# Kernel optimization log

Hardware: AMD Instinct MI355X
Metric: run time of the kernel (lower is better)

The kernel has to match this reference:

```python
import jax, jax.numpy as jnp
import numpy as np

B, T, C = 16, 1024, 32
PATCH_SIZE = 4
NB_PATCHES = 400
STRETCH = 8
K = PATCH_SIZE * C          # patch_size * num_channels = 128
S_MAIN = T // STRETCH       # 128 strided steps for the main layer
P_TOP = max(int(0.15 * NB_PATCHES), PATCH_SIZE - 1)  # 60 ontop patches


def setup_inputs() -> dict:
    key = jax.random.key(0)
    k0, k1, k2, k3, k4 = jax.random.split(key, 5)
    x = jax.random.normal(k0, (B, T, C), dtype=jnp.float32)
    # flattened (time*C + channel) gather indices, stand-in for the
    # precomputed random (time, channel) pairs used by tf.gather_nd
    idx_main = jax.random.randint(k1, (S_MAIN, NB_PATCHES, K), 0, T * C, dtype=jnp.int32)
    idx_top = jax.random.randint(k2, (T, P_TOP, K), 0, T * C, dtype=jnp.int32)
    W_main = jax.random.normal(k3, (S_MAIN, NB_PATCHES, K), dtype=jnp.float32) * 0.05
    b_main = jnp.zeros((S_MAIN, NB_PATCHES), dtype=jnp.float32)
    W_top = jax.random.normal(k4, (T, P_TOP, K), dtype=jnp.float32) * 0.05
    b_top = jnp.zeros((T, P_TOP), dtype=jnp.float32)
    return {"x": x, "W_main": W_main, "b_main": b_main,
            "W_top": W_top, "b_top": b_top,
            "idx_main": idx_main, "idx_top": idx_top}


def reference(x, W_main, b_main, W_top, b_top, idx_main, idx_top):
    # x: [B, T, C] -> flatten time/channel plane for gather (== gather_nd on [T, C, B])
    Bsz, Tlen, Cch = x.shape
    flat = x.reshape(Bsz, Tlen * Cch)                      # [B, T*C]
    # main strided patches: [B, S_MAIN, NB_PATCHES, K]
    Mm = jnp.take(flat, idx_main.reshape(-1), axis=1).reshape(Bsz, *idx_main.shape)
    out_main = jax.nn.leaky_relu(
        jnp.einsum('bspk,spk->bsp', Mm, W_main) + b_main, 0.3)  # [B, S_MAIN, P]
    # upsample strided steps back to full sequence (tf_repeat along time)
    stretch = Tlen // idx_main.shape[0]
    out_main = jnp.repeat(out_main, stretch, axis=1)            # [B, T, P]
    # ontop patches at every step: [B, T, P_TOP, K]
    Mt = jnp.take(flat, idx_top.reshape(-1), axis=1).reshape(Bsz, *idx_top.shape)
    out_top = jax.nn.leaky_relu(
        jnp.einsum('btpk,tpk->btp', Mt, W_top) + b_top, 0.3)    # [B, T, P_TOP]
    return jnp.concatenate([out_main, out_top], axis=-1)       # [B, T, P + P_TOP]
```

## Files before the change

### kernel.cpp

```cpp
#include <hip/hip_runtime.h>

#define B_SZ    16
#define T_LEN   1024
#define C_CH    32
#define TC      (T_LEN * C_CH)
#define S_MAIN  128
#define NB_P    400
#define P_TOP   60
#define KDIM    128
#define STRETCH 8
#define OUT_CH  (NB_P + P_TOP)

__global__ __launch_bounds__(256) void transpose_x(const float* __restrict__ x,
                                                   float* __restrict__ xT) {
    __shared__ float tile[16][129];
    const int i0 = blockIdx.x * 128;
    const int t  = threadIdx.x;
    #pragma unroll
    for (int r = 0; r < 8; ++r) {
        int e  = r * 256 + t;
        int b  = e >> 7;
        int ii = e & 127;
        tile[b][ii] = x[b * TC + i0 + ii];
    }
    __syncthreads();
    #pragma unroll
    for (int r = 0; r < 8; ++r) {
        int e  = r * 256 + t;
        int ii = e >> 4;
        int b  = e & 15;
        xT[i0 * 16 + e] = tile[b][ii];
    }
}

__device__ __forceinline__ float4 fma4(float4 a, float s, float4 g) {
    a.x += g.x * s; a.y += g.y * s; a.z += g.z * s; a.w += g.w * s;
    return a;
}

template <int NPAIR_P, int NROWS, bool TO_WS>
__global__ __launch_bounds__(256) void patch_kernel(
    const float* __restrict__ xT,
    const int*   __restrict__ idx,
    const float* __restrict__ W,
    const float* __restrict__ bias,
    float*       __restrict__ dst)
{
    const int wave = threadIdx.x >> 6;
    const int lane = threadIdx.x & 63;
    const int pair = blockIdx.x * 4 + wave;
    const int j    = lane >> 2;
    const int bq   = lane & 3;

    const int4*   idx4 = (const int4*)idx + (size_t)pair * 32 + j * 2;
    const float4* w4   = (const float4*)W  + (size_t)pair * 32 + j * 2;
    const float4* xT4  = (const float4*)xT;

    const int4   ia = idx4[0];
    const int4   ib = idx4[1];
    const float4 wa = w4[0];
    const float4 wb = w4[1];

    float4 acc = make_float4(0.f, 0.f, 0.f, 0.f);
    acc = fma4(acc, wa.x, xT4[ia.x * 4 + bq]);
    acc = fma4(acc, wa.y, xT4[ia.y * 4 + bq]);
    acc = fma4(acc, wa.z, xT4[ia.z * 4 + bq]);
    acc = fma4(acc, wa.w, xT4[ia.w * 4 + bq]);
    acc = fma4(acc, wb.x, xT4[ib.x * 4 + bq]);
    acc = fma4(acc, wb.y, xT4[ib.y * 4 + bq]);
    acc = fma4(acc, wb.z, xT4[ib.z * 4 + bq]);
    acc = fma4(acc, wb.w, xT4[ib.w * 4 + bq]);

    #pragma unroll
    for (int mask = 4; mask <= 32; mask <<= 1) {
        acc.x += __shfl_xor(acc.x, mask);
        acc.y += __shfl_xor(acc.y, mask);
        acc.z += __shfl_xor(acc.z, mask);
        acc.w += __shfl_xor(acc.w, mask);
    }

    if (j == 0) {
        const float bv = bias[pair];
        const int row = pair / NPAIR_P;
        const int p   = pair - row * NPAIR_P;
        float v[4] = {acc.x, acc.y, acc.z, acc.w};
        #pragma unroll
        for (int m = 0; m < 4; ++m) {
            const int b = bq * 4 + m;
            float val = v[m] + bv;
            val = (val > 0.f) ? val : 0.3f * val;
            if (TO_WS) {
                dst[((size_t)b * NROWS + row) * NPAIR_P + p] = val;
            } else {
                dst[((size_t)b * T_LEN + row) * OUT_CH + NB_P + p] = val;
            }
        }
    }
}

__global__ __launch_bounds__(256) void upsample_main(const float* __restrict__ ws_main,
                                                     float* __restrict__ out) {
    const int o4 = blockIdx.x * 256 + threadIdx.x;
    const int row = o4 / 100;
    const int col = o4 - row * 100;
    const int b = row >> 10;
    const int t = row & 1023;
    const int s = t >> 3;
    const float4 v = ((const float4*)ws_main)[((size_t)b * S_MAIN + s) * 100 + col];
    ((float4*)out)[(size_t)row * 115 + col] = v;
}

extern "C" void kernel_launch(void* const* d_in, const int* in_sizes, int n_in,
                              void* d_out, int out_size, void* d_ws, size_t ws_size,
                              hipStream_t stream) {
    const float* x      = (const float*)d_in[0];
    const float* W_main = (const float*)d_in[1];
    const float* b_main = (const float*)d_in[2];
    const float* W_top  = (const float*)d_in[3];
    const float* b_top  = (const float*)d_in[4];
    const int*  idx_main = (const int*)d_in[5];
    const int*  idx_top  = (const int*)d_in[6];
    float* out = (float*)d_out;

    float* xT      = (float*)d_ws;
    float* ws_main = (float*)((char*)d_ws + (size_t)TC * 16 * 4);

    transpose_x<<<TC / 128, 256, 0, stream>>>(x, xT);

    patch_kernel<NB_P, S_MAIN, true>
        <<<(S_MAIN * NB_P) / 4, 256, 0, stream>>>(xT, idx_main, W_main, b_main, ws_main);

    patch_kernel<P_TOP, T_LEN, false>
        <<<(T_LEN * P_TOP) / 4, 256, 0, stream>>>(xT, idx_top, W_top, b_top, out);

    upsample_main<<<(B_SZ * T_LEN * 100) / 256, 256, 0, stream>>>(ws_main, out);
}
```

Baseline: 260.1 us.

## Pack transposed input as bf16 and process four patches per wave via LDS staging

The transpose now converts x to bf16 and packs all 16 batch values of a flat index into 32 bytes, which halves the size of every random gather. Each wave now handles four patch pairs, staging their index and weight rows in shared memory with nontemporal loads. Each lane gathers 16 bytes covering 8 batches and accumulates in fp32. Output and upsample writes use nontemporal stores. Rounding x to bf16 adds precision loss to the results, and the larger per-lane accumulator raises register pressure.

```diff
diff --git a/kernel.cpp b/kernel.cpp
--- a/kernel.cpp
+++ b/kernel.cpp
@@ -7,92 +7,117 @@
 #define S_MAIN  128
 #define NB_P    400
 #define P_TOP   60
-#define KDIM    128
-#define STRETCH 8
 #define OUT_CH  (NB_P + P_TOP)
 
-__global__ __launch_bounds__(256) void transpose_x(const float* __restrict__ x,
-                                                   float* __restrict__ xT) {
-    __shared__ float tile[16][129];
-    const int i0 = blockIdx.x * 128;
-    const int t  = threadIdx.x;
-    #pragma unroll
-    for (int r = 0; r < 8; ++r) {
-        int e  = r * 256 + t;
-        int b  = e >> 7;
-        int ii = e & 127;
-        tile[b][ii] = x[b * TC + i0 + ii];
-    }
-    __syncthreads();
-    #pragma unroll
-    for (int r = 0; r < 8; ++r) {
-        int e  = r * 256 + t;
-        int ii = e >> 4;
-        int b  = e & 15;
-        xT[i0 * 16 + e] = tile[b][ii];
-    }
+typedef float        v4f __attribute__((ext_vector_type(4)));
+typedef int          v4i __attribute__((ext_vector_type(4)));
+typedef unsigned int v4u __attribute__((ext_vector_type(4)));
+
+__device__ __forceinline__ unsigned short f32_to_bf16_rne(float f) {
+    unsigned int u = __float_as_uint(f);
+    unsigned int r = u + 0x7fffu + ((u >> 16) & 1u);
+    return (unsigned short)(r >> 16);
 }
 
-__device__ __forceinline__ float4 fma4(float4 a, float s, float4 g) {
-    a.x += g.x * s; a.y += g.y * s; a.z += g.z * s; a.w += g.w * s;
-    return a;
+__global__ __launch_bounds__(256) void transpose_pack(const float* __restrict__ x,
+                                                      unsigned int* __restrict__ xb) {
+    const int i = blockIdx.x * 256 + threadIdx.x;
+    unsigned int u[8];
+    #pragma unroll
+    for (int k = 0; k < 8; ++k) {
+        float v0 = __builtin_nontemporal_load(x + (size_t)(2 * k)     * TC + i);
+        float v1 = __builtin_nontemporal_load(x + (size_t)(2 * k + 1) * TC + i);
+        u[k] = (unsigned int)f32_to_bf16_rne(v0) |
+               ((unsigned int)f32_to_bf16_rne(v1) << 16);
+    }
+    v4u a = { u[0], u[1], u[2], u[3] };
+    v4u b = { u[4], u[5], u[6], u[7] };
+    v4u* out = (v4u*)xb;
+    out[(size_t)i * 2]     = a;
+    out[(size_t)i * 2 + 1] = b;
 }
 
 template <int NPAIR_P, int NROWS, bool TO_WS>
-__global__ __launch_bounds__(256) void patch_kernel(
-    const float* __restrict__ xT,
+__global__ __launch_bounds__(256, 4) void patch_v3(
+    const v4u*   __restrict__ xb4,
     const int*   __restrict__ idx,
     const float* __restrict__ W,
     const float* __restrict__ bias,
     float*       __restrict__ dst)
 {
+    __shared__ int   s_idx[16][128];
+    __shared__ float s_w[16][128];
     const int wave = threadIdx.x >> 6;
     const int lane = threadIdx.x & 63;
-    const int pair = blockIdx.x * 4 + wave;
-    const int j    = lane >> 2;
-    const int bq   = lane & 3;
-
-    const int4*   idx4 = (const int4*)idx + (size_t)pair * 32 + j * 2;
-    const float4* w4   = (const float4*)W  + (size_t)pair * 32 + j * 2;
-    const float4* xT4  = (const float4*)xT;
-
-    const int4   ia = idx4[0];
-    const int4   ib = idx4[1];
-    const float4 wa = w4[0];
-    const float4 wb = w4[1];
-
-    float4 acc = make_float4(0.f, 0.f, 0.f, 0.f);
-    acc = fma4(acc, wa.x, xT4[ia.x * 4 + bq]);
-    acc = fma4(acc, wa.y, xT4[ia.y * 4 + bq]);
-    acc = fma4(acc, wa.z, xT4[ia.z * 4 + bq]);
-    acc = fma4(acc, wa.w, xT4[ia.w * 4 + bq]);
-    acc = fma4(acc, wb.x, xT4[ib.x * 4 + bq]);
-    acc = fma4(acc, wb.y, xT4[ib.y * 4 + bq]);
-    acc = fma4(acc, wb.z, xT4[ib.z * 4 + bq]);
-    acc = fma4(acc, wb.w, xT4[ib.w * 4 + bq]);
+    const int pairBase = blockIdx.x * 16 + wave * 4;
 
     #pragma unroll
-    for (int mask = 4; mask <= 32; mask <<= 1) {
-        acc.x += __shfl_xor(acc.x, mask);
-        acc.y += __shfl_xor(acc.y, mask);
-        acc.z += __shfl_xor(acc.z, mask);
-        acc.w += __shfl_xor(acc.w, mask);
+    for (int q = 0; q < 4; ++q) {
+        const int pr = pairBase + q;
+        if (lane < 32) {
+            v4i t = __builtin_nontemporal_load((const v4i*)idx + (size_t)pr * 32 + lane);
+            *(v4i*)&s_idx[wave * 4 + q][lane * 4] = t;
+        } else {
+            v4f t = __builtin_nontemporal_load((const v4f*)W + (size_t)pr * 32 + (lane - 32));
+            *(v4f*)&s_w[wave * 4 + q][(lane - 32) * 4] = t;
+        }
     }
 
+    const int j  = lane >> 1;
+    const int bh = lane & 1;
+
+    float acc[4][8];
+    #pragma unroll
+    for (int q = 0; q < 4; ++q)
+        #pragma unroll
+        for (int k = 0; k < 8; ++k) acc[q][k] = 0.f;
+
+    float bv[4];
+
+    #pragma unroll
+    for (int q = 0; q < 4; ++q) {
+        bv[q] = bias[pairBase + q];
+        #pragma unroll
+        for (int g = 0; g < 4; ++g) {
+            const int   ix = s_idx[wave * 4 + q][g * 32 + j];
+            const float wt = s_w [wave * 4 + q][g * 32 + j];
+            const v4u gv = xb4[(size_t)ix * 2 + bh];
+            acc[q][0] += __uint_as_float(gv.x << 16)          * wt;
+            acc[q][1] += __uint_as_float(gv.x & 0xffff0000u)  * wt;
+            acc[q][2] += __uint_as_float(gv.y << 16)          * wt;
+            acc[q][3] += __uint_as_float(gv.y & 0xffff0000u)  * wt;
+            acc[q][4] += __uint_as_float(gv.z << 16)          * wt;
+            acc[q][5] += __uint_as_float(gv.z & 0xffff0000u)  * wt;
+            acc[q][6] += __uint_as_float(gv.w << 16)          * wt;
+            acc[q][7] += __uint_as_float(gv.w & 0xffff0000u)  * wt;
+        }
+    }
+
+    #pragma unroll
+    for (int q = 0; q < 4; ++q)
+        #pragma unroll
+        for (int m = 2; m <= 32; m <<= 1)
+            #pragma unroll
+            for (int k = 0; k < 8; ++k)
+                acc[q][k] += __shfl_xor(acc[q][k], m);
+
     if (j == 0) {
-        const float bv = bias[pair];
-        const int row = pair / NPAIR_P;
-        const int p   = pair - row * NPAIR_P;
-        float v[4] = {acc.x, acc.y, acc.z, acc.w};
         #pragma unroll
-        for (int m = 0; m < 4; ++m) {
-            const int b = bq * 4 + m;
-            float val = v[m] + bv;
-            val = (val > 0.f) ? val : 0.3f * val;
-            if (TO_WS) {
-                dst[((size_t)b * NROWS + row) * NPAIR_P + p] = val;
-            } else {
-                dst[((size_t)b * T_LEN + row) * OUT_CH + NB_P + p] = val;
+        for (int q = 0; q < 4; ++q) {
+            const int pr  = pairBase + q;
+            const int row = pr / NPAIR_P;
+            const int p   = pr - row * NPAIR_P;
+            #pragma unroll
+            for (int k = 0; k < 8; ++k) {
+                const int b = bh * 8 + k;
+                float val = acc[q][k] + bv[q];
+                val = (val > 0.f) ? val : 0.3f * val;
+                if (TO_WS) {
+                    dst[((size_t)b * NROWS + row) * NPAIR_P + p] = val;
+                } else {
+                    __builtin_nontemporal_store(
+                        val, &dst[((size_t)b * T_LEN + row) * OUT_CH + NB_P + p]);
+                }
             }
         }
     }
@@ -106,8 +131,8 @@
     const int b = row >> 10;
     const int t = row & 1023;
     const int s = t >> 3;
-    const float4 v = ((const float4*)ws_main)[((size_t)b * S_MAIN + s) * 100 + col];
-    ((float4*)out)[(size_t)row * 115 + col] = v;
+    const v4f v = ((const v4f*)ws_main)[((size_t)b * S_MAIN + s) * 100 + col];
+    __builtin_nontemporal_store(v, &((v4f*)out)[(size_t)row * 115 + col]);
 }
 
 extern "C" void kernel_launch(void* const* d_in, const int* in_sizes, int n_in,
@@ -122,16 +147,16 @@
     const int*  idx_top  = (const int*)d_in[6];
     float* out = (float*)d_out;
 
-    float* xT      = (float*)d_ws;
-    float* ws_main = (float*)((char*)d_ws + (size_t)TC * 16 * 4);
+    unsigned int* xb   = (unsigned int*)d_ws;
+    float* ws_main     = (float*)((char*)d_ws + (size_t)TC * 16 * 2);
 
-    transpose_x<<<TC / 128, 256, 0, stream>>>(x, xT);
+    transpose_pack<<<TC / 256, 256, 0, stream>>>(x, xb);
 
-    patch_kernel<NB_P, S_MAIN, true>
-        <<<(S_MAIN * NB_P) / 4, 256, 0, stream>>>(xT, idx_main, W_main, b_main, ws_main);
+    patch_v3<NB_P, S_MAIN, true>
+        <<<(S_MAIN * NB_P) / 16, 256, 0, stream>>>((const v4u*)xb, idx_main, W_main, b_main, ws_main);
 
-    patch_kernel<P_TOP, T_LEN, false>
-        <<<(T_LEN * P_TOP) / 4, 256, 0, stream>>>(xT, idx_top, W_top, b_top, out);
+    patch_v3<P_TOP, T_LEN, false>
+        <<<(T_LEN * P_TOP) / 16, 256, 0, stream>>>((const v4u*)xb, idx_top, W_top, b_top, out);
 
     upsample_main<<<(B_SZ * T_LEN * 100) / 256, 256, 0, stream>>>(ws_main, out);
 }
```

Result: slower. 274.2 us (+5.4%).

## Stage bf16-packed batch pairs in LDS and gather from shared memory

Applied to the files above, without the earlier changes.

The input x is converted to bf16 with two batch elements packed per 32-bit word, split into 8 batch-pair groups. Each 1024-thread block loads one group's full time-channel plane (128 KB) into LDS and then loops over a chunk of patch pairs, gathering from LDS instead of doing scattered global float4 reads. This aims to replace random global and L2 gathers with LDS gathers. In exchange it reads idx and W 8 times (once per group), lowers input precision to bf16, and runs only one block per CU because of the large LDS footprint.

```diff
diff --git a/kernel.cpp b/kernel.cpp
--- a/kernel.cpp
+++ b/kernel.cpp
@@ -7,92 +7,108 @@
 #define S_MAIN  128
 #define NB_P    400
 #define P_TOP   60
-#define KDIM    128
-#define STRETCH 8
 #define OUT_CH  (NB_P + P_TOP)
+#define NGROUP  8
 
-__global__ __launch_bounds__(256) void transpose_x(const float* __restrict__ x,
-                                                   float* __restrict__ xT) {
-    __shared__ float tile[16][129];
-    const int i0 = blockIdx.x * 128;
-    const int t  = threadIdx.x;
+typedef float        v4f __attribute__((ext_vector_type(4)));
+typedef unsigned int v4u __attribute__((ext_vector_type(4)));
+
+__device__ __forceinline__ unsigned short f32_to_bf16_rne(float f) {
+    unsigned int u = __float_as_uint(f);
+    unsigned int r = u + 0x7fffu + ((u >> 16) & 1u);
+    return (unsigned short)(r >> 16);
+}
+
+__global__ __launch_bounds__(256) void transpose_pack(const float* __restrict__ x,
+                                                      unsigned int* __restrict__ xs) {
+    const int i = blockIdx.x * 256 + threadIdx.x;
     #pragma unroll
-    for (int r = 0; r < 8; ++r) {
-        int e  = r * 256 + t;
-        int b  = e >> 7;
-        int ii = e & 127;
-        tile[b][ii] = x[b * TC + i0 + ii];
-    }
-    __syncthreads();
-    #pragma unroll
-    for (int r = 0; r < 8; ++r) {
-        int e  = r * 256 + t;
-        int ii = e >> 4;
-        int b  = e & 15;
-        xT[i0 * 16 + e] = tile[b][ii];
+    for (int g = 0; g < NGROUP; ++g) {
+        float v0 = x[(size_t)(2 * g)     * TC + i];
+        float v1 = x[(size_t)(2 * g + 1) * TC + i];
+        unsigned int u = (unsigned int)f32_to_bf16_rne(v0) |
+                         ((unsigned int)f32_to_bf16_rne(v1) << 16);
+        xs[(size_t)g * TC + i] = u;
     }
 }
 
-__device__ __forceinline__ float4 fma4(float4 a, float s, float4 g) {
-    a.x += g.x * s; a.y += g.y * s; a.z += g.z * s; a.w += g.w * s;
-    return a;
+__device__ __forceinline__ float leaky(float v) {
+    return (v > 0.f) ? v : 0.3f * v;
 }
 
-template <int NPAIR_P, int NROWS, bool TO_WS>
-__global__ __launch_bounds__(256) void patch_kernel(
-    const float* __restrict__ xT,
+template <int NPAIR_P, int NROWS, int NCHUNK, bool TO_WS>
+__global__ __launch_bounds__(1024, 1) void patch_lds(
+    const unsigned int* __restrict__ xs,
     const int*   __restrict__ idx,
     const float* __restrict__ W,
     const float* __restrict__ bias,
     float*       __restrict__ dst)
 {
+    __shared__ unsigned int s_x[TC];
+    constexpr int NPAIRS = NPAIR_P * NROWS;
+    constexpr int CHUNK  = NPAIRS / NCHUNK;
+
+    const int bI = blockIdx.x;
+    const int r  = bI >> 3;
+    const int g  = r & 7;
+    const int c  = (bI & 7) + 8 * (r >> 3);
+
+    {
+        const v4u* src = (const v4u*)(xs + (size_t)g * TC);
+        v4u* dl = (v4u*)s_x;
+        const int t = threadIdx.x;
+        #pragma unroll
+        for (int k = 0; k < 8; ++k)
+            dl[k * 1024 + t] = src[k * 1024 + t];
+    }
+    __syncthreads();
+
     const int wave = threadIdx.x >> 6;
     const int lane = threadIdx.x & 63;
-    const int pair = blockIdx.x * 4 + wave;
+    const int q    = lane & 3;
     const int j    = lane >> 2;
-    const int bq   = lane & 3;
 
-    const int4*   idx4 = (const int4*)idx + (size_t)pair * 32 + j * 2;
-    const float4* w4   = (const float4*)W  + (size_t)pair * 32 + j * 2;
-    const float4* xT4  = (const float4*)xT;
+    const int pair_lo = c * CHUNK;
+    const int pair_hi = pair_lo + CHUNK;
 
-    const int4   ia = idx4[0];
-    const int4   ib = idx4[1];
-    const float4 wa = w4[0];
-    const float4 wb = w4[1];
+    for (int p0 = pair_lo + wave * 4; p0 < pair_hi; p0 += 64) {
+        const int pair = p0 + q;
 
-    float4 acc = make_float4(0.f, 0.f, 0.f, 0.f);
-    acc = fma4(acc, wa.x, xT4[ia.x * 4 + bq]);
-    acc = fma4(acc, wa.y, xT4[ia.y * 4 + bq]);
-    acc = fma4(acc, wa.z, xT4[ia.z * 4 + bq]);
-    acc = fma4(acc, wa.w, xT4[ia.w * 4 + bq]);
-    acc = fma4(acc, wb.x, xT4[ib.x * 4 + bq]);
-    acc = fma4(acc, wb.y, xT4[ib.y * 4 + bq]);
-    acc = fma4(acc, wb.z, xT4[ib.z * 4 + bq]);
-    acc = fma4(acc, wb.w, xT4[ib.w * 4 + bq]);
+        const int4*   i4 = (const int4*)(idx + (size_t)pair * 128 + j * 8);
+        const v4f*    w4 = (const v4f*)  (W   + (size_t)pair * 128 + j * 8);
+        const int4 ia = i4[0];
+        const int4 ib = i4[1];
+        const v4f  wa = w4[0];
+        const v4f  wb = w4[1];
 
-    #pragma unroll
-    for (int mask = 4; mask <= 32; mask <<= 1) {
-        acc.x += __shfl_xor(acc.x, mask);
-        acc.y += __shfl_xor(acc.y, mask);
-        acc.z += __shfl_xor(acc.z, mask);
-        acc.w += __shfl_xor(acc.w, mask);
-    }
+        float a0 = 0.f, a1 = 0.f;
+        #define GATHER(IX, WT)                                        \
+            { unsigned int gv = s_x[(IX)];                            \
+              a0 += __uint_as_float(gv << 16)         * (WT);         \
+              a1 += __uint_as_float(gv & 0xffff0000u) * (WT); }
+        GATHER(ia.x, wa.x) GATHER(ia.y, wa.y) GATHER(ia.z, wa.z) GATHER(ia.w, wa.w)
+        GATHER(ib.x, wb.x) GATHER(ib.y, wb.y) GATHER(ib.z, wb.z) GATHER(ib.w, wb.w)
+        #undef GATHER
 
-    if (j == 0) {
-        const float bv = bias[pair];
-        const int row = pair / NPAIR_P;
-        const int p   = pair - row * NPAIR_P;
-        float v[4] = {acc.x, acc.y, acc.z, acc.w};
         #pragma unroll
-        for (int m = 0; m < 4; ++m) {
-            const int b = bq * 4 + m;
-            float val = v[m] + bv;
-            val = (val > 0.f) ? val : 0.3f * val;
+        for (int m = 4; m <= 32; m <<= 1) {
+            a0 += __shfl_xor(a0, m);
+            a1 += __shfl_xor(a1, m);
+        }
+
+        if (j == 0) {
+            const float bv = bias[pair];
+            const int row = pair / NPAIR_P;
+            const int p   = pair - row * NPAIR_P;
+            const float v0 = leaky(a0 + bv);
+            const float v1 = leaky(a1 + bv);
+            const int b0 = 2 * g, b1 = 2 * g + 1;
             if (TO_WS) {
-                dst[((size_t)b * NROWS + row) * NPAIR_P + p] = val;
+                dst[((size_t)b0 * NROWS + row) * NPAIR_P + p] = v0;
+                dst[((size_t)b1 * NROWS + row) * NPAIR_P + p] = v1;
             } else {
-                dst[((size_t)b * T_LEN + row) * OUT_CH + NB_P + p] = val;
+                dst[((size_t)b0 * T_LEN + row) * OUT_CH + NB_P + p] = v0;
+                dst[((size_t)b1 * T_LEN + row) * OUT_CH + NB_P + p] = v1;
             }
         }
     }
@@ -106,8 +122,8 @@
     const int b = row >> 10;
     const int t = row & 1023;
     const int s = t >> 3;
-    const float4 v = ((const float4*)ws_main)[((size_t)b * S_MAIN + s) * 100 + col];
-    ((float4*)out)[(size_t)row * 115 + col] = v;
+    const v4f v = ((const v4f*)ws_main)[((size_t)b * S_MAIN + s) * 100 + col];
+    ((v4f*)out)[(size_t)row * 115 + col] = v;
 }
 
 extern "C" void kernel_launch(void* const* d_in, const int* in_sizes, int n_in,
@@ -122,16 +138,16 @@
     const int*  idx_top  = (const int*)d_in[6];
     float* out = (float*)d_out;
 
-    float* xT      = (float*)d_ws;
-    float* ws_main = (float*)((char*)d_ws + (size_t)TC * 16 * 4);
+    unsigned int* xs  = (unsigned int*)d_ws;
+    float* ws_main    = (float*)((char*)d_ws + (size_t)NGROUP * TC * 4);
 
-    transpose_x<<<TC / 128, 256, 0, stream>>>(x, xT);
+    transpose_pack<<<TC / 256, 256, 0, stream>>>(x, xs);
 
-    patch_kernel<NB_P, S_MAIN, true>
-        <<<(S_MAIN * NB_P) / 4, 256, 0, stream>>>(xT, idx_main, W_main, b_main, ws_main);
+    patch_lds<NB_P, S_MAIN, 64, true>
+        <<<64 * NGROUP, 1024, 0, stream>>>(xs, idx_main, W_main, b_main, ws_main);
 
-    patch_kernel<P_TOP, T_LEN, false>
-        <<<(T_LEN * P_TOP) / 4, 256, 0, stream>>>(xT, idx_top, W_top, b_top, out);
+    patch_lds<P_TOP, T_LEN, 64, false>
+        <<<64 * NGROUP, 1024, 0, stream>>>(xs, idx_top, W_top, b_top, out);
 
     upsample_main<<<(B_SZ * T_LEN * 100) / 256, 256, 0, stream>>>(ws_main, out);
 }
```

Result: faster. 252.6 us (-2.9%).
